# Optimization experiments

Measured on AMD Instinct MI355X. Metric: run time of the kernel, lower is better.

The kernel has to match this reference:

```python
import jax, jax.numpy as jnp
import numpy as np

EPS = 1e-12  # F.normalize eps


def sage_conv(x, src, dst, n_nodes, W_l, b_l, W_r):
    """PyG SAGEConv with mean aggregation and L2 normalize.
    out = lin_l(mean_{j in N(i)} x_j) + lin_r(x_i), then row-wise L2 normalize.
    """
    # mean-aggregate neighbor features: scatter-add then divide by in-degree
    msg_sum = jax.ops.segment_sum(x[src], dst, num_segments=n_nodes)  # [N, F]
    deg = jax.ops.segment_sum(jnp.ones_like(dst, dtype=x.dtype), dst,
                              num_segments=n_nodes)                   # [N]
    agg = msg_sum / jnp.maximum(deg, 1.0)[:, None]
    out = agg @ W_l + b_l + x @ W_r                                   # [N, out]
    norm = jnp.sqrt(jnp.sum(out * out, axis=-1, keepdims=True))
    return out / jnp.maximum(norm, EPS)


def setup_inputs() -> dict:
    key = jax.random.key(0)
    ks = jax.random.split(key, 8)
    N, E, D_IN, D_H, D_OUT = 100000, 320000, 256, 64, 4
    x = jax.random.normal(ks[0], (N, D_IN), dtype=jnp.float32)
    edge_index = jax.random.randint(ks[1], (2, E), 0, N, dtype=jnp.int32)
    s1 = 1.0 / np.sqrt(D_IN)
    s2 = 1.0 / np.sqrt(D_H)
    W1_l = jax.random.uniform(ks[2], (D_IN, D_H), jnp.float32, -s1, s1)
    b1_l = jnp.zeros((D_H,), jnp.float32)
    W1_r = jax.random.uniform(ks[3], (D_IN, D_H), jnp.float32, -s1, s1)
    W2_l = jax.random.uniform(ks[4], (D_H, D_OUT), jnp.float32, -s2, s2)
    b2_l = jnp.zeros((D_OUT,), jnp.float32)
    W2_r = jax.random.uniform(ks[5], (D_H, D_OUT), jnp.float32, -s2, s2)
    return {"x": x, "edge_index": edge_index,
            "W1_l": W1_l, "b1_l": b1_l, "W1_r": W1_r,
            "W2_l": W2_l, "b2_l": b2_l, "W2_r": W2_r}


def reference(x, edge_index, W1_l, b1_l, W1_r, W2_l, b2_l, W2_r):
    # eval mode: dropout is identity
    n_nodes = x.shape[0]
    src, dst = edge_index[0], edge_index[1]
    h = jax.nn.relu(sage_conv(x, src, dst, n_nodes, W1_l, b1_l, W1_r))
    out = sage_conv(h, src, dst, n_nodes, W2_l, b2_l, W2_r)
    return out
```

## Files before the change

kernel.cpp:

```cpp
#include <hip/hip_runtime.h>

#define DIN 256
#define DH  64
#define DOUT 4
#define CAP 32

typedef __attribute__((ext_vector_type(8))) short bf16x8;
typedef __attribute__((ext_vector_type(4))) float f32x4;

__device__ __forceinline__ short f2bf(float f) {
    unsigned int u = __float_as_uint(f);
    unsigned int r = (u + 0x7FFFu + ((u >> 16) & 1u)) >> 16;
    return (short)r;
}
__device__ __forceinline__ short f2bf_trunc(float f) {
    return (short)(__float_as_uint(f) >> 16);
}
__device__ __forceinline__ float bf2f(short h) {
    return __uint_as_float(((unsigned int)(unsigned short)h) << 16);
}

__global__ void fillprep_kernel(const int* __restrict__ src, const int* __restrict__ dst,
                                int* __restrict__ cnt, int* __restrict__ bucket,
                                const float* __restrict__ Wl, const float* __restrict__ Wr,
                                short* __restrict__ WTh, short* __restrict__ WTl,
                                int E, int FB)
{
    if ((int)blockIdx.x >= FB) {
        const int n = blockIdx.x - FB;
        const int k = threadIdx.x;
        const float v = (n < 64) ? Wl[k * 64 + n] : Wr[k * 64 + (n - 64)];
        const short hi = f2bf(v);
        const short lo = f2bf(v - bf2f(hi));
        WTh[n * 256 + k] = hi;
        WTl[n * 256 + k] = lo;
        return;
    }
    const int e = blockIdx.x * 256 + threadIdx.x;
    if (e >= E) return;
    const int d = dst[e];
    const int p = atomicAdd(&cnt[d], 1);
    if (p < CAP) bucket[(size_t)d * CAP + p] = src[e];
}

#define XS_LD 40
__device__ __forceinline__ void cvt_store8(const float4& a, const float4& b,
                                           short* dh, short* dl) {
    bf16x8 ph, pl;
    float fv[8] = {a.x, a.y, a.z, a.w, b.x, b.y, b.z, b.w};
    #pragma unroll
    for (int j = 0; j < 8; ++j) {
        const short hi = f2bf_trunc(fv[j]);
        ph[j] = hi;
        pl[j] = f2bf_trunc(fv[j] - bf2f(hi));
    }
    *(bf16x8*)dh = ph;
    *(bf16x8*)dl = pl;
}

__global__ __launch_bounds__(256, 4) void gemm1_mfma(
    const float* __restrict__ x, const short* __restrict__ WTh,
    const short* __restrict__ WTl, float* __restrict__ y, int N)
{
    __shared__ short xsh[2][64 * XS_LD];
    __shared__ short xsl[2][64 * XS_LD];

    const int tid  = threadIdx.x;
    const int wave = tid >> 6;
    const int lane = tid & 63;
    const int lm   = lane & 15;
    const int quad = lane >> 4;
    const int brow = blockIdx.x * 64;

    const int xr    = tid >> 2;
    const int xk    = (tid & 3) * 8;
    const int row_g = brow + xr;
    const bool xvalid = (row_g < N);
    const float* xptr = x + (size_t)row_g * DIN + xk;
    const int xs_off = xr * XS_LD + xk;

    const int col0 = wave * 32 + lm;
    const size_t wb0 = (size_t)col0 * 256 + quad * 8;
    const size_t wb1 = (size_t)(col0 + 16) * 256 + quad * 8;

    f32x4 acc[4][2];
    #pragma unroll
    for (int mt = 0; mt < 4; ++mt)
        #pragma unroll
        for (int nt = 0; nt < 2; ++nt)
            acc[mt][nt] = (f32x4){0.f, 0.f, 0.f, 0.f};

    float4 sA0, sB0, sA1, sB1;
    sA0 = sB0 = sA1 = sB1 = make_float4(0.f, 0.f, 0.f, 0.f);
    if (xvalid) {
        sA0 = ((const float4*)xptr)[0];
        sB0 = ((const float4*)xptr)[1];
        sA1 = ((const float4*)(xptr + 32))[0];
        sB1 = ((const float4*)(xptr + 32))[1];
    }
    bf16x8 wh_cur[2], wl_cur[2];
    wh_cur[0] = *(const bf16x8*)(WTh + wb0);
    wh_cur[1] = *(const bf16x8*)(WTh + wb1);
    wl_cur[0] = *(const bf16x8*)(WTl + wb0);
    wl_cur[1] = *(const bf16x8*)(WTl + wb1);

    cvt_store8(sA0, sB0, &xsh[0][xs_off], &xsl[0][xs_off]);
    if (xvalid) {
        sA0 = ((const float4*)(xptr + 64))[0];
        sB0 = ((const float4*)(xptr + 64))[1];
    }
    asm volatile("s_waitcnt lgkmcnt(0)" ::: "memory");
    __builtin_amdgcn_s_barrier();

    #pragma unroll
    for (int k = 0; k < 8; ++k) {
        const int buf = k & 1;

        bf16x8 wh_nxt[2], wl_nxt[2];
        if (k < 7) {
            if ((k & 1) == 0)
                cvt_store8(sA1, sB1, &xsh[buf ^ 1][xs_off], &xsl[buf ^ 1][xs_off]);
            else
                cvt_store8(sA0, sB0, &xsh[buf ^ 1][xs_off], &xsl[buf ^ 1][xs_off]);
            if (k < 5 && xvalid) {
                const int kc = (k + 3) * 32;
                if ((k & 1) == 0) {
                    sA1 = ((const float4*)(xptr + kc))[0];
                    sB1 = ((const float4*)(xptr + kc))[1];
                } else {
                    sA0 = ((const float4*)(xptr + kc))[0];
                    sB0 = ((const float4*)(xptr + kc))[1];
                }
            }
            const int kc1 = (k + 1) * 32;
            wh_nxt[0] = *(const bf16x8*)(WTh + wb0 + kc1);
            wh_nxt[1] = *(const bf16x8*)(WTh + wb1 + kc1);
            wl_nxt[0] = *(const bf16x8*)(WTl + wb0 + kc1);
            wl_nxt[1] = *(const bf16x8*)(WTl + wb1 + kc1);
        }

        #pragma unroll
        for (int mt = 0; mt < 4; ++mt) {
            const int aoff = (mt * 16 + lm) * XS_LD + quad * 8;
            const bf16x8 ah = *(const bf16x8*)(&xsh[buf][aoff]);
            const bf16x8 al = *(const bf16x8*)(&xsl[buf][aoff]);
            #pragma unroll
            for (int nt = 0; nt < 2; ++nt) {
                acc[mt][nt] = __builtin_amdgcn_mfma_f32_16x16x32_bf16(
                    ah, wh_cur[nt], acc[mt][nt], 0, 0, 0);
                acc[mt][nt] = __builtin_amdgcn_mfma_f32_16x16x32_bf16(
                    ah, wl_cur[nt], acc[mt][nt], 0, 0, 0);
                acc[mt][nt] = __builtin_amdgcn_mfma_f32_16x16x32_bf16(
                    al, wh_cur[nt], acc[mt][nt], 0, 0, 0);
            }
        }

        if (k < 7) {
            #pragma unroll
            for (int nt = 0; nt < 2; ++nt) {
                wh_cur[nt] = wh_nxt[nt];
                wl_cur[nt] = wl_nxt[nt];
            }
            asm volatile("s_waitcnt lgkmcnt(0)" ::: "memory");
            __builtin_amdgcn_s_barrier();
        }
    }

    #pragma unroll
    for (int mt = 0; mt < 4; ++mt) {
        #pragma unroll
        for (int r = 0; r < 4; ++r) {
            const int rg = brow + mt * 16 + quad * 4 + r;
            if (rg < N) {
                const int col = wave * 32 + lm;
                float* yp = y + (size_t)rg * 128 + col;
                yp[0]  = acc[mt][0][r];
                yp[16] = acc[mt][1][r];
            }
        }
    }
}

__global__ __launch_bounds__(256) void fused1_kernel(
    const float* __restrict__ y, const int* __restrict__ cnt, const int* __restrict__ bucket,
    const float* __restrict__ b1, const float* __restrict__ W2l, const float* __restrict__ W2r,
    float* __restrict__ z, int N)
{
    const int wave = threadIdx.x >> 6;
    const int lane = threadIdx.x & 63;
    const int i = blockIdx.x * 4 + wave;
    if (i >= N) return;

    const int deg = cnt[i];
    const int dd = (deg < CAP) ? deg : CAP;

    int myn = (lane < dd) ? bucket[(size_t)i * CAP + lane] : 0;

    float acc = 0.f;
    int j = 0;
    for (; j + 1 < dd; j += 2) {
        const int s0 = __shfl(myn, j, 64);
        const int s1 = __shfl(myn, j + 1, 64);
        const float v0 = y[(size_t)s0 * 128 + lane];
        const float v1 = y[(size_t)s1 * 128 + lane];
        acc += v0 + v1;
    }
    if (j < dd) {
        const int s0 = __shfl(myn, j, 64);
        acc += y[(size_t)s0 * 128 + lane];
    }

    const float dinv = 1.0f / fmaxf((float)deg, 1.0f);
    float v = acc * dinv + b1[lane] + y[(size_t)i * 128 + 64 + lane];

    float ss = v * v;
    #pragma unroll
    for (int m = 32; m >= 1; m >>= 1) ss += __shfl_xor(ss, m, 64);
    const float inv = 1.0f / fmaxf(sqrtf(ss), 1e-12f);
    const float hv = fmaxf(v * inv, 0.f);

    const float4 wl = *(const float4*)(W2l + lane * 4);
    const float4 wr = *(const float4*)(W2r + lane * 4);
    float p0 = hv * wl.x, p1 = hv * wl.y, p2 = hv * wl.z, p3 = hv * wl.w;
    float p4 = hv * wr.x, p5 = hv * wr.y, p6 = hv * wr.z, p7 = hv * wr.w;

    const bool b0 = (lane & 1) != 0;
    float s0_ = b0 ? p0 : p4;
    float s1_ = b0 ? p1 : p5;
    float s2_ = b0 ? p2 : p6;
    float s3_ = b0 ? p3 : p7;
    float q0 = (b0 ? p4 : p0) + __shfl_xor(s0_, 1, 64);
    float q1 = (b0 ? p5 : p1) + __shfl_xor(s1_, 1, 64);
    float q2 = (b0 ? p6 : p2) + __shfl_xor(s2_, 1, 64);
    float q3 = (b0 ? p7 : p3) + __shfl_xor(s3_, 1, 64);
    const bool b1b = (lane & 2) != 0;
    float t0 = b1b ? q0 : q2;
    float t1 = b1b ? q1 : q3;
    float r0 = (b1b ? q2 : q0) + __shfl_xor(t0, 2, 64);
    float r1 = (b1b ? q3 : q1) + __shfl_xor(t1, 2, 64);
    const bool b2 = (lane & 4) != 0;
    float u0 = b2 ? r0 : r1;
    float zv = (b2 ? r1 : r0) + __shfl_xor(u0, 4, 64);
    zv += __shfl_xor(zv, 8, 64);
    zv += __shfl_xor(zv, 16, 64);
    zv += __shfl_xor(zv, 32, 64);
    const int ch = 4 * (lane & 1) + ((lane & 2)) + ((lane >> 2) & 1);
    if (lane < 8) z[(size_t)i * 8 + ch] = zv;
}

__global__ void fused2_kernel(const float* __restrict__ z, const int* __restrict__ cnt,
                              const int* __restrict__ bucket, const float* __restrict__ b2,
                              float* __restrict__ out, int N)
{
    const int i = blockIdx.x * blockDim.x + threadIdx.x;
    if (i >= N) return;
    const int deg = cnt[i];
    const int dd = (deg < CAP) ? deg : CAP;
    float4 acc = make_float4(0.f, 0.f, 0.f, 0.f);
    for (int j = 0; j < dd; ++j) {
        const int s = bucket[(size_t)i * CAP + j];
        const float4 t = *(const float4*)(z + (size_t)s * 8);
        acc.x += t.x; acc.y += t.y; acc.z += t.z; acc.w += t.w;
    }
    const float dinv = 1.0f / fmaxf((float)deg, 1.0f);
    const float4 r  = *(const float4*)(z + (size_t)i * 8 + 4);
    const float4 bb = *(const float4*)(b2);
    float4 o;
    o.x = acc.x * dinv + bb.x + r.x;
    o.y = acc.y * dinv + bb.y + r.y;
    o.z = acc.z * dinv + bb.z + r.z;
    o.w = acc.w * dinv + bb.w + r.w;
    const float ss = o.x * o.x + o.y * o.y + o.z * o.z + o.w * o.w;
    const float inv = 1.0f / fmaxf(sqrtf(ss), 1e-12f);
    o.x *= inv; o.y *= inv; o.z *= inv; o.w *= inv;
    *(float4*)(out + (size_t)i * 4) = o;
}

extern "C" void kernel_launch(void* const* d_in, const int* in_sizes, int n_in,
                              void* d_out, int out_size, void* d_ws, size_t ws_size,
                              hipStream_t stream)
{
    const float* x    = (const float*)d_in[0];
    const int*   ei   = (const int*)d_in[1];
    const float* W1l  = (const float*)d_in[2];
    const float* b1l  = (const float*)d_in[3];
    const float* W1r  = (const float*)d_in[4];
    const float* W2l  = (const float*)d_in[5];
    const float* b2l  = (const float*)d_in[6];
    const float* W2r  = (const float*)d_in[7];
    float* out = (float*)d_out;

    const int N = in_sizes[0] / DIN;
    const int E = in_sizes[1] / 2;
    const int* src = ei;
    const int* dst = ei + E;

    char* ws = (char*)d_ws;
    size_t woff = 0;
    auto alloc = [&](size_t bytes) {
        void* p = ws + woff;
        woff += (bytes + 255) & ~(size_t)255;
        return p;
    };
    float* y      = (float*)alloc((size_t)N * 128 * 4);
    float* z      = (float*)alloc((size_t)N * 8 * 4);
    short* WTh    = (short*)alloc((size_t)128 * 256 * 2);
    short* WTl    = (short*)alloc((size_t)128 * 256 * 2);
    int*   cnt    = (int*)alloc((size_t)N * 4);
    int*   bucket = (int*)alloc((size_t)N * CAP * 4);

    hipMemsetAsync(cnt, 0, (size_t)N * 4, stream);

    const int FB = (E + 255) / 256;
    fillprep_kernel<<<FB + 128, 256, 0, stream>>>(src, dst, cnt, bucket,
                                                  W1l, W1r, WTh, WTl, E, FB);

    gemm1_mfma<<<(N + 63) / 64, 256, 0, stream>>>(x, WTh, WTl, y, N);

    fused1_kernel<<<(N + 3) / 4, 256, 0, stream>>>(y, cnt, bucket, b1l, W2l, W2r, z, N);

    fused2_kernel<<<(N + 255) / 256, 256, 0, stream>>>(z, cnt, bucket, b2l, out, N);
}
```

Baseline: 268.9 us.

## Stage x tiles via global_load_lds with 4-deep LDS ring in gemm1

Replaces the register-staged x loads in the first-layer GEMM with direct global-to-LDS async loads into a 4-slot raw fp32 ring buffer. Each chunk is then converted from LDS into the bf16 hi/lo split tiles. Hand-tuned vmcnt waits keep up to four chunks in flight. This aims to hide global memory latency better and free registers. In exchange it adds 32KB of LDS per block, lowers the occupancy hint to 3, and relies on fragile manual waitcnt accounting.

```diff
diff --git a/kernel.cpp b/kernel.cpp
--- a/kernel.cpp
+++ b/kernel.cpp
@@ -6,6 +6,7 @@
 #define CAP 32
 
 typedef __attribute__((ext_vector_type(8))) short bf16x8;
+typedef __attribute__((ext_vector_type(4))) short bf16x4;
 typedef __attribute__((ext_vector_type(4))) float f32x4;
 
 __device__ __forceinline__ short f2bf(float f) {
@@ -44,24 +45,24 @@
 }
 
 #define XS_LD 40
-__device__ __forceinline__ void cvt_store8(const float4& a, const float4& b,
-                                           short* dh, short* dl) {
-    bf16x8 ph, pl;
-    float fv[8] = {a.x, a.y, a.z, a.w, b.x, b.y, b.z, b.w};
+
+__device__ __forceinline__ void cvt_split4(const float4 v, bf16x4* ph, bf16x4* pl) {
+    bf16x4 h, l;
+    float fv[4] = {v.x, v.y, v.z, v.w};
     #pragma unroll
-    for (int j = 0; j < 8; ++j) {
-        const short hi = f2bf_trunc(fv[j]);
-        ph[j] = hi;
-        pl[j] = f2bf_trunc(fv[j] - bf2f(hi));
-    }
-    *(bf16x8*)dh = ph;
-    *(bf16x8*)dl = pl;
-}
-
-__global__ __launch_bounds__(256, 4) void gemm1_mfma(
+    for (int c = 0; c < 4; ++c) {
+        const short hi = f2bf_trunc(fv[c]);
+        h[c] = hi;
+        l[c] = f2bf_trunc(fv[c] - bf2f(hi));
+    }
+    *ph = h; *pl = l;
+}
+
+__global__ __launch_bounds__(256, 3) void gemm1_mfma(
     const float* __restrict__ x, const short* __restrict__ WTh,
     const short* __restrict__ WTl, float* __restrict__ y, int N)
 {
+    __shared__ float rawx[4][2048];
     __shared__ short xsh[2][64 * XS_LD];
     __shared__ short xsl[2][64 * XS_LD];
 
@@ -72,12 +73,15 @@
     const int quad = lane >> 4;
     const int brow = blockIdx.x * 64;
 
-    const int xr    = tid >> 2;
-    const int xk    = (tid & 3) * 8;
-    const int row_g = brow + xr;
-    const bool xvalid = (row_g < N);
-    const float* xptr = x + (size_t)row_g * DIN + xk;
-    const int xs_off = xr * XS_LD + xk;
+    const int srow  = wave * 16 + (lane >> 3);
+    const int scolF = (lane & 7) * 4;
+    const float* gs0 = x + (size_t)min(brow + srow,     N - 1) * DIN + scolF;
+    const float* gs1 = x + (size_t)min(brow + srow + 8, N - 1) * DIN + scolF;
+    const int ldsb  = wave * 512;
+
+    const int cvt_base = wave * 512 + lane * 4;
+    const int crow0 = wave * 16 + (lane >> 3);
+    const int ccol  = (lane & 7) * 4;
 
     const int col0 = wave * 32 + lm;
     const size_t wb0 = (size_t)col0 * 256 + quad * 8;
@@ -90,81 +94,98 @@
         for (int nt = 0; nt < 2; ++nt)
             acc[mt][nt] = (f32x4){0.f, 0.f, 0.f, 0.f};
 
-    float4 sA0, sB0, sA1, sB1;
-    sA0 = sB0 = sA1 = sB1 = make_float4(0.f, 0.f, 0.f, 0.f);
-    if (xvalid) {
-        sA0 = ((const float4*)xptr)[0];
-        sB0 = ((const float4*)xptr)[1];
-        sA1 = ((const float4*)(xptr + 32))[0];
-        sB1 = ((const float4*)(xptr + 32))[1];
-    }
-    bf16x8 wh_cur[2], wl_cur[2];
+    bf16x8 wh_cur[2], wl_cur[2], wh_nxt[2], wl_nxt[2];
+
+#define STAGE_CHUNK(cc)                                                          \
+    {                                                                            \
+        constexpr int sl_ = (cc) & 3;                                            \
+        __builtin_amdgcn_global_load_lds(                                        \
+            (const __attribute__((address_space(1))) unsigned int*)(gs0 + (cc) * 32), \
+            (__attribute__((address_space(3))) unsigned int*)&rawx[sl_][ldsb],   \
+            16, 0, 0);                                                           \
+        __builtin_amdgcn_global_load_lds(                                        \
+            (const __attribute__((address_space(1))) unsigned int*)(gs1 + (cc) * 32), \
+            (__attribute__((address_space(3))) unsigned int*)&rawx[sl_][ldsb + 256], \
+            16, 0, 0);                                                           \
+    }
+
+#define CONVERT_CHUNK(cc, bb)                                                    \
+    {                                                                            \
+        constexpr int sl_ = (cc) & 3;                                            \
+        const float4 r0 = *(const float4*)&rawx[sl_][cvt_base];                  \
+        const float4 r1 = *(const float4*)&rawx[sl_][cvt_base + 256];            \
+        bf16x4 h0, l0, h1, l1;                                                   \
+        cvt_split4(r0, &h0, &l0);                                                \
+        cvt_split4(r1, &h1, &l1);                                                \
+        *(bf16x4*)&xsh[bb][crow0 * XS_LD + ccol] = h0;                           \
+        *(bf16x4*)&xsl[bb][crow0 * XS_LD + ccol] = l0;                           \
+        *(bf16x4*)&xsh[bb][(crow0 + 8) * XS_LD + ccol] = h1;                     \
+        *(bf16x4*)&xsl[bb][(crow0 + 8) * XS_LD + ccol] = l1;                     \
+    }
+
+    STAGE_CHUNK(0) STAGE_CHUNK(1) STAGE_CHUNK(2) STAGE_CHUNK(3)
     wh_cur[0] = *(const bf16x8*)(WTh + wb0);
     wh_cur[1] = *(const bf16x8*)(WTh + wb1);
     wl_cur[0] = *(const bf16x8*)(WTl + wb0);
     wl_cur[1] = *(const bf16x8*)(WTl + wb1);
-
-    cvt_store8(sA0, sB0, &xsh[0][xs_off], &xsl[0][xs_off]);
-    if (xvalid) {
-        sA0 = ((const float4*)(xptr + 64))[0];
-        sB0 = ((const float4*)(xptr + 64))[1];
-    }
+    asm volatile("s_waitcnt vmcnt(6)" ::: "memory");
+    CONVERT_CHUNK(0, 0)
     asm volatile("s_waitcnt lgkmcnt(0)" ::: "memory");
     __builtin_amdgcn_s_barrier();
-
-    #pragma unroll
-    for (int k = 0; k < 8; ++k) {
-        const int buf = k & 1;
-
-        bf16x8 wh_nxt[2], wl_nxt[2];
-        if (k < 7) {
-            if ((k & 1) == 0)
-                cvt_store8(sA1, sB1, &xsh[buf ^ 1][xs_off], &xsl[buf ^ 1][xs_off]);
-            else
-                cvt_store8(sA0, sB0, &xsh[buf ^ 1][xs_off], &xsl[buf ^ 1][xs_off]);
-            if (k < 5 && xvalid) {
-                const int kc = (k + 3) * 32;
-                if ((k & 1) == 0) {
-                    sA1 = ((const float4*)(xptr + kc))[0];
-                    sB1 = ((const float4*)(xptr + kc))[1];
-                } else {
-                    sA0 = ((const float4*)(xptr + kc))[0];
-                    sB0 = ((const float4*)(xptr + kc))[1];
-                }
-            }
-            const int kc1 = (k + 1) * 32;
-            wh_nxt[0] = *(const bf16x8*)(WTh + wb0 + kc1);
-            wh_nxt[1] = *(const bf16x8*)(WTh + wb1 + kc1);
-            wl_nxt[0] = *(const bf16x8*)(WTl + wb0 + kc1);
-            wl_nxt[1] = *(const bf16x8*)(WTl + wb1 + kc1);
-        }
-
-        #pragma unroll
-        for (int mt = 0; mt < 4; ++mt) {
-            const int aoff = (mt * 16 + lm) * XS_LD + quad * 8;
-            const bf16x8 ah = *(const bf16x8*)(&xsh[buf][aoff]);
-            const bf16x8 al = *(const bf16x8*)(&xsl[buf][aoff]);
-            #pragma unroll
-            for (int nt = 0; nt < 2; ++nt) {
-                acc[mt][nt] = __builtin_amdgcn_mfma_f32_16x16x32_bf16(
-                    ah, wh_cur[nt], acc[mt][nt], 0, 0, 0);
-                acc[mt][nt] = __builtin_amdgcn_mfma_f32_16x16x32_bf16(
-                    ah, wl_cur[nt], acc[mt][nt], 0, 0, 0);
-                acc[mt][nt] = __builtin_amdgcn_mfma_f32_16x16x32_bf16(
-                    al, wh_cur[nt], acc[mt][nt], 0, 0, 0);
-            }
-        }
-
-        if (k < 7) {
-            #pragma unroll
-            for (int nt = 0; nt < 2; ++nt) {
-                wh_cur[nt] = wh_nxt[nt];
-                wl_cur[nt] = wl_nxt[nt];
-            }
-            asm volatile("s_waitcnt lgkmcnt(0)" ::: "memory");
-            __builtin_amdgcn_s_barrier();
-        }
-    }
+    __builtin_amdgcn_sched_barrier(0);
+
+#define GEMM_ITER(K, NK_STR)                                                     \
+    {                                                                            \
+        constexpr int k_ = (K);                                                  \
+        constexpr int buf_ = k_ & 1;                                             \
+        if (k_ < 7) {                                                            \
+            const int kc1 = (k_ + 1) * 32;                                       \
+            wh_nxt[0] = *(const bf16x8*)(WTh + wb0 + kc1);                       \
+            wh_nxt[1] = *(const bf16x8*)(WTh + wb1 + kc1);                       \
+            wl_nxt[0] = *(const bf16x8*)(WTl + wb0 + kc1);                       \
+            wl_nxt[1] = *(const bf16x8*)(WTl + wb1 + kc1);                       \
+        }                                                                        \
+        if (k_ < 4) STAGE_CHUNK(k_ + 4)                                          \
+        if (k_ < 7) {                                                            \
+            asm volatile("s_waitcnt vmcnt(" NK_STR ")" ::: "memory");            \
+            CONVERT_CHUNK(k_ + 1, buf_ ^ 1)                                      \
+        }                                                                        \
+        _Pragma("unroll")                                                        \
+        for (int mt = 0; mt < 4; ++mt) {                                         \
+            const int aoff = (mt * 16 + lm) * XS_LD + quad * 8;                  \
+            const bf16x8 ah = *(const bf16x8*)(&xsh[buf_][aoff]);                \
+            const bf16x8 al = *(const bf16x8*)(&xsl[buf_][aoff]);                \
+            _Pragma("unroll")                                                    \
+            for (int nt = 0; nt < 2; ++nt) {                                     \
+                acc[mt][nt] = __builtin_amdgcn_mfma_f32_16x16x32_bf16(           \
+                    ah, wh_cur[nt], acc[mt][nt], 0, 0, 0);                       \
+                acc[mt][nt] = __builtin_amdgcn_mfma_f32_16x16x32_bf16(           \
+                    ah, wl_cur[nt], acc[mt][nt], 0, 0, 0);                       \
+                acc[mt][nt] = __builtin_amdgcn_mfma_f32_16x16x32_bf16(           \
+                    al, wh_cur[nt], acc[mt][nt], 0, 0, 0);                       \
+            }                                                                    \
+        }                                                                        \
+        if (k_ < 7) {                                                            \
+            wh_cur[0] = wh_nxt[0]; wh_cur[1] = wh_nxt[1];                        \
+            wl_cur[0] = wl_nxt[0]; wl_cur[1] = wl_nxt[1];                        \
+            asm volatile("s_waitcnt lgkmcnt(0)" ::: "memory");                   \
+            __builtin_amdgcn_s_barrier();                                        \
+            __builtin_amdgcn_sched_barrier(0);                                   \
+        }                                                                        \
+    }
+
+    GEMM_ITER(0, "10")
+    GEMM_ITER(1, "14")
+    GEMM_ITER(2, "18")
+    GEMM_ITER(3, "18")
+    GEMM_ITER(4, "16")
+    GEMM_ITER(5, "14")
+    GEMM_ITER(6, "12")
+    GEMM_ITER(7, "0")
+
+#undef GEMM_ITER
+#undef CONVERT_CHUNK
+#undef STAGE_CHUNK
 
     #pragma unroll
     for (int mt = 0; mt < 4; ++mt) {
```

Result: no change. 265.5 us (-1.3%).
